# Kernel tuning notes

Measured on AMD Instinct MI355X. Metric: run time of the kernel, lower is better.

Reference implementation:

```python
import jax, jax.numpy as jnp
import numpy as np

EPS = 1e-15

def gmm_conv(x, row, col, pseudo, g_w, mu, sigma, root_w, bias):
    # x: [N,Fin], pseudo: [E,D], g_w: [Fin,K*Fout], mu/sigma: [K,D], root_w: [Fin,Fout]
    N = x.shape[0]
    K, D = mu.shape
    Fout = g_w.shape[1] // K
    gx = (x @ g_w).reshape(N, K, Fout)                       # per-node kernel transforms
    diff = pseudo[:, None, :] - mu[None, :, :]               # [E,K,D]
    gauss = jnp.exp(-0.5 * jnp.sum(diff * diff / (EPS + sigma[None] ** 2), axis=-1))  # [E,K]
    msg = jnp.einsum('ek,eko->eo', gauss, gx[row])           # [E,Fout]
    agg = jax.ops.segment_sum(msg, col, num_segments=N)      # scatter-add to targets
    cnt = jax.ops.segment_sum(jnp.ones((msg.shape[0],), x.dtype), col, num_segments=N)
    agg = agg / jnp.maximum(cnt, 1.0)[:, None]               # mean aggregation (GMMConv default)
    return agg + x @ root_w + bias

def setup_inputs() -> dict:
    key = jax.random.key(0)
    ks = jax.random.split(key, 12)
    N, E, F, H, C, K, D = 50000, 800000, 128, 64, 16, 8, 2
    return {
        'x': jax.random.normal(ks[0], (N, F), jnp.float32),
        'edge_index': jax.random.randint(ks[1], (2, E), 0, N, jnp.int64),
        'edge_attr': jax.random.uniform(ks[2], (E, D), jnp.float32),
        'g1_w': jax.random.normal(ks[3], (F, K * H), jnp.float32) * 0.1,
        'mu1': jax.random.normal(ks[4], (K, D), jnp.float32),
        'sigma1': jax.random.uniform(ks[5], (K, D), jnp.float32) + 0.5,
        'root1_w': jax.random.normal(ks[6], (F, H), jnp.float32) * 0.1,
        'bias1': jnp.zeros((H,), jnp.float32),
        'g2_w': jax.random.normal(ks[7], (H, K * C), jnp.float32) * 0.1,
        'mu2': jax.random.normal(ks[8], (K, D), jnp.float32),
        'sigma2': jax.random.uniform(ks[9], (K, D), jnp.float32) + 0.5,
        'root2_w': jax.random.normal(ks[10], (H, C), jnp.float32) * 0.1,
        'bias2': jnp.zeros((C,), jnp.float32),
    }

def reference(x, edge_index, edge_attr, g1_w, mu1, sigma1, root1_w, bias1,
              g2_w, mu2, sigma2, root2_w, bias2):
    row, col = edge_index[0], edge_index[1]
    # dropout p applied in eval mode -> identity
    h = jax.nn.elu(gmm_conv(x, row, col, edge_attr, g1_w, mu1, sigma1, root1_w, bias1))
    out = gmm_conv(h, row, col, edge_attr, g2_w, mu2, sigma2, root2_w, bias2)
    return jax.nn.log_softmax(out, axis=1)
```

## Files before the change

### kernel.cpp

```cpp
#include <hip/hip_runtime.h>
#include <hip/hip_bf16.h>
#include <hip/hip_fp16.h>
#include <math.h>


#define NF 128
#define NH 64
#define NC 16
#define Z1NODES 16
#define Z1CAP 448
#define E2NODES 16
#define E2CAP 448
#define GXST 160

typedef __bf16 v8bf __attribute__((ext_vector_type(8)));
typedef float v4f __attribute__((ext_vector_type(4)));
typedef float v2f __attribute__((ext_vector_type(2)));

__device__ inline ushort f2bu(float x) {
  __hip_bfloat16 h = __float2bfloat16(x);
  return *(ushort*)&h;
}
__device__ inline v8bf ld_frag(const ushort* p) {
  uint4 u = *(const uint4*)p;
  return __builtin_bit_cast(v8bf, u);
}
__device__ inline v2f fma2(float w, v2f f, v2f a) {
  return __builtin_elementwise_fma((v2f){w, w}, f, a);
}

__global__ __launch_bounds__(256) void setup_kernel(
    const int* __restrict__ col, const float* __restrict__ x,
    const float* __restrict__ g1w, const float* __restrict__ r1w,
    const float* __restrict__ g2w, const float* __restrict__ r2w,
    int* __restrict__ counts, int* __restrict__ rank,
    ushort* __restrict__ A1, ushort* __restrict__ W1t,
    ushort* __restrict__ G2pT, int* __restrict__ bagg,
    int E, int N, int bh, int bc, int bp) {
  const int b = blockIdx.x, t = threadIdx.x;
  if (b < bh) {
    int e = b * 256 + t;
    if (e < E) rank[e] = atomicAdd(&counts[col[e]], 1);
  } else if (b < bh + bc) {
    int idx = (b - bh) * 256 + t;
    if (idx < N * 32) {
      int n = idx >> 5, c4 = idx & 31;
      float4 v = ((const float4*)x)[idx];
      ushort4 o;
      o.x = f2bu(v.x); o.y = f2bu(v.y); o.z = f2bu(v.z); o.w = f2bu(v.w);
      *(ushort4*)(A1 + (size_t)n * 1152 + 1024 + c4 * 4) = o;
    }
  } else if (b < bh + bc + bp) {
    int i = (b - bh - bc) * 256 + t;
    if (i < 64 * 1152) {
      int h = i / 1152, j = i % 1152;
      float v = (j < 1024) ? g1w[(size_t)(j & 127) * 512 + (j >> 7) * 64 + h]
                           : r1w[(size_t)(j - 1024) * 64 + h];
      W1t[i] = f2bu(v);
    } else {
      int i2 = i - 64 * 1152;
      if (i2 < 144 * 64) {
        int cp = i2 / 64, f = i2 % 64;
        float v;
        if (cp < 128) {
          int kq = cp >> 5, rem = cp & 31;
          int o = rem >> 1, k = kq * 2 + (rem & 1);
          v = g2w[(size_t)f * 128 + k * 16 + o];
        } else {
          v = r2w[(size_t)f * 16 + (cp - 128)];
        }
        G2pT[i2] = f2bu(v);
      }
    }
  } else {
    if (t < 64) bagg[t] = 0;
  }
}

__global__ __launch_bounds__(256) void scan_kernel(
    const int* __restrict__ counts, int* __restrict__ starts,
    int* __restrict__ bagg, int NB) {
  __shared__ int wsum[4];
  __shared__ int s_pre;
  const int t = threadIdx.x, lane = t & 63, wv = t >> 6;
  const int b = blockIdx.x;
  int4 v = ((const int4*)counts)[b * 256 + t];
  int tsum = v.x + v.y + v.z + v.w;
  int inc = tsum;
  #pragma unroll
  for (int off = 1; off < 64; off <<= 1) {
    int u = __shfl_up(inc, off, 64);
    if (lane >= off) inc += u;
  }
  if (lane == 63) wsum[wv] = inc;
  __syncthreads();
  int agg = wsum[0] + wsum[1] + wsum[2] + wsum[3];
  if (t == 0) atomicExch(&bagg[b], agg + 1);
  __threadfence();
  int pre = 0;
  if (wv == 0) {
    if (t < b) {
      int val;
      do { val = atomicAdd(&bagg[t], 0); } while (val == 0);
      pre = val - 1;
    }
    #pragma unroll
    for (int off = 32; off >= 1; off >>= 1) pre += __shfl_xor(pre, off, 64);
    if (lane == 0) s_pre = pre;
  }
  __syncthreads();
  int wpre = 0;
  for (int j = 0; j < wv; ++j) wpre += wsum[j];
  int excl = s_pre + wpre + inc - tsum;
  int4 o;
  o.x = excl; o.y = o.x + v.x; o.z = o.y + v.y; o.w = o.z + v.z;
  ((int4*)starts)[b * 256 + t] = o;
}

__global__ __launch_bounds__(256) void fillrec_kernel(
    const int* __restrict__ row, const int* __restrict__ col,
    const int* __restrict__ rank, const int* __restrict__ starts,
    const float* __restrict__ eattr, uint4* __restrict__ rec, int E) {
  int e = blockIdx.x * 256 + threadIdx.x;
  if (e >= E) return;
  int pos = starts[col[e]] + rank[e];
  int r = row[e];
  float2 p = *(const float2*)(eattr + 2 * e);
  rec[pos] = make_uint4((uint)(r * 2304), __float_as_uint(p.x),
                        __float_as_uint(p.y), (uint)(r * 320));
}

__global__ __launch_bounds__(256) void z1_kernel(
    ushort* __restrict__ A1, const uint4* __restrict__ rec,
    const float* __restrict__ mu1, const float* __restrict__ sg1,
    const int* __restrict__ starts, int N) {
  __shared__ __align__(16) float lw[Z1CAP + 8][8];
  __shared__ int loff[Z1CAP + 8];
  __shared__ float prm[32];
  const int t = threadIdx.x, lane = t & 63, wv = t >> 6;
  const int base = (int)blockIdx.x * Z1NODES;
  const int S = starts[base];
  const int cl = min(starts[base + Z1NODES] - S, Z1CAP);
  if (t < 8) {
    float s0 = sg1[2 * t], s1 = sg1[2 * t + 1];
    prm[t] = -0.5f / (1e-15f + s0 * s0);
    prm[8 + t] = -0.5f / (1e-15f + s1 * s1);
    prm[16 + t] = mu1[2 * t];
    prm[24 + t] = mu1[2 * t + 1];
  }
  __syncthreads();
  for (int i = t; i < cl; i += 256) {
    uint4 rr = rec[S + i];
    loff[i] = (int)rr.x;
    float p0 = __uint_as_float(rr.y), p1 = __uint_as_float(rr.z);
    float w[8];
    #pragma unroll
    for (int k = 0; k < 8; ++k) {
      float d0 = p0 - prm[16 + k], d1 = p1 - prm[24 + k];
      w[k] = __expf(fmaf(d0 * d0, prm[k], d1 * d1 * prm[8 + k]));
    }
    *(float4*)&lw[i][0] = make_float4(w[0], w[1], w[2], w[3]);
    *(float4*)&lw[i][4] = make_float4(w[4], w[5], w[6], w[7]);
  }
  if (t < 8) {
    loff[cl + t] = 0;
    *(float4*)&lw[cl + t][0] = make_float4(0.f, 0.f, 0.f, 0.f);
    *(float4*)&lw[cl + t][4] = make_float4(0.f, 0.f, 0.f, 0.f);
  }
  __syncthreads();

  const char* xb = (const char*)(A1 + 1024) + (lane << 2);

  for (int i = 0; i < Z1NODES / 4; ++i) {
    const int n = base + wv * 4 + i;
    const int be = starts[n], ee = starts[n + 1];
    v2f A[8];
    #pragma unroll
    for (int k = 0; k < 8; ++k) A[k] = (v2f){0.f, 0.f};

    const int reRel = min(ee - S, cl);
    for (int q = min(be - S, cl); q < reRel; q += 8) {
      int off[8];
      #pragma unroll
      for (int u = 0; u < 8; ++u) off[u] = loff[q + u];
      uint g[8];
      #pragma unroll
      for (int u = 0; u < 8; ++u) g[u] = *(const uint*)(xb + off[u]);
      #pragma unroll
      for (int u = 0; u < 8; ++u) {
        const bool ok = (q + u) < reRel;
        float4 wl = *(float4*)&lw[q + u][0];
        float4 wh = *(float4*)&lw[q + u][4];
        v2f F;
        F.x = ok ? __uint_as_float(g[u] << 16) : 0.f;
        F.y = ok ? __uint_as_float(g[u] & 0xffff0000u) : 0.f;
        A[0] = fma2(wl.x, F, A[0]);
        A[1] = fma2(wl.y, F, A[1]);
        A[2] = fma2(wl.z, F, A[2]);
        A[3] = fma2(wl.w, F, A[3]);
        A[4] = fma2(wh.x, F, A[4]);
        A[5] = fma2(wh.y, F, A[5]);
        A[6] = fma2(wh.z, F, A[6]);
        A[7] = fma2(wh.w, F, A[7]);
      }
    }
    const float inv = 1.f / fmaxf((float)(ee - be), 1.f);
    ushort* zr = A1 + (size_t)n * 1152;
    #pragma unroll
    for (int k = 0; k < 8; ++k) {
      uint pk = (uint)f2bu(A[k].x * inv) | ((uint)f2bu(A[k].y * inv) << 16);
      *(uint*)(zr + k * 128 + 2 * lane) = pk;
    }
  }
}

__global__ __launch_bounds__(256) void gemm12_kernel(
    const ushort* __restrict__ A1, const ushort* __restrict__ W1t,
    const float* __restrict__ b1, const ushort* __restrict__ G2pT,
    ushort* __restrict__ gx2e, int N) {
  __shared__ __align__(16) ushort As[2][64 * 32];
  __shared__ __align__(16) ushort Bs[2][64 * 32];
  __shared__ __align__(16) ushort Hs[64][72];
  const int t = threadIdx.x, lane = t & 63, wv = t >> 6;
  const int mfrag = lane & 15, quad = lane >> 4;
  const int m0 = (int)blockIdx.x * 64;
  const int st_r = t >> 2, st_c = (t & 3) * 8;
  const int st_o = st_r * 32 + st_c;
  const ushort* ag = A1 + (size_t)(m0 + st_r) * 1152 + st_c;
  const ushort* bg = W1t + (size_t)st_r * 1152 + st_c;

  {
    uint4 a0 = *(const uint4*)ag;
    uint4 b0 = *(const uint4*)bg;
    *(uint4*)(&As[0][st_o]) = a0;
    *(uint4*)(&Bs[0][st_o]) = b0;
  }
  __syncthreads();

  v4f acc[4];
  #pragma unroll
  for (int ct = 0; ct < 4; ++ct) acc[ct] = (v4f){0.f, 0.f, 0.f, 0.f};

  for (int kc = 0; kc < 36; ++kc) {
    const int cb = kc & 1, nb = cb ^ 1;
    uint4 an, bn;
    if (kc < 35) {
      an = *(const uint4*)(ag + (kc + 1) * 32);
      bn = *(const uint4*)(bg + (kc + 1) * 32);
    }
    v8bf a = ld_frag(&As[cb][(wv * 16 + mfrag) * 32 + quad * 8]);
    #pragma unroll
    for (int ct = 0; ct < 4; ++ct) {
      v8bf b = ld_frag(&Bs[cb][(ct * 16 + mfrag) * 32 + quad * 8]);
      acc[ct] = __builtin_amdgcn_mfma_f32_16x16x32_bf16(a, b, acc[ct], 0, 0, 0);
    }
    if (kc < 35) {
      *(uint4*)(&As[nb][st_o]) = an;
      *(uint4*)(&Bs[nb][st_o]) = bn;
      __syncthreads();
    }
  }
  #pragma unroll
  for (int ct = 0; ct < 4; ++ct) {
    const int colh = ct * 16 + mfrag;
    const float bc = b1[colh];
    #pragma unroll
    for (int r = 0; r < 4; ++r) {
      float v = acc[ct][r] + bc;
      v = v > 0.f ? v : expm1f(v);
      Hs[wv * 16 + quad * 4 + r][colh] = f2bu(v);
    }
  }
  __syncthreads();

  v4f acc2[9];
  #pragma unroll
  for (int t9 = 0; t9 < 9; ++t9) acc2[t9] = (v4f){0.f, 0.f, 0.f, 0.f};
  const ushort* brow = G2pT + (size_t)mfrag * 64 + quad * 8;
  #pragma unroll
  for (int kc = 0; kc < 2; ++kc) {
    v8bf a = ld_frag(&Hs[wv * 16 + mfrag][quad * 8 + kc * 32]);
    #pragma unroll
    for (int t9 = 0; t9 < 9; ++t9) {
      v8bf b = ld_frag(brow + (size_t)t9 * 16 * 64 + kc * 32);
      acc2[t9] = __builtin_amdgcn_mfma_f32_16x16x32_bf16(a, b, acc2[t9], 0, 0, 0);
    }
  }
  #pragma unroll
  for (int t9 = 0; t9 < 9; ++t9) {
    #pragma unroll
    for (int r = 0; r < 4; ++r) {
      int node = m0 + wv * 16 + quad * 4 + r;
      if (node < N)
        gx2e[(size_t)node * GXST + t9 * 16 + mfrag] = f2bu(acc2[t9][r]);
    }
  }
}

__global__ __launch_bounds__(256) void edge2_kernel(
    const ushort* __restrict__ gx2e, const uint4* __restrict__ rec,
    const float* __restrict__ mu2, const float* __restrict__ sg2,
    const int* __restrict__ starts, const float* __restrict__ b2,
    float* __restrict__ out, int N) {
  __shared__ __align__(16) float lw[E2CAP + 8][8];
  __shared__ int loff[E2CAP + 8];
  __shared__ float lb2[16];
  __shared__ float prm[32];
  const int t = threadIdx.x, lane = t & 63, wv = t >> 6;
  const int base = (int)blockIdx.x * E2NODES;
  const int S = starts[base];
  const int cl = min(starts[base + E2NODES] - S, E2CAP);
  if (t < 16) lb2[t] = b2[t];
  if (t < 8) {
    float s0 = sg2[2 * t], s1 = sg2[2 * t + 1];
    prm[t] = -0.5f / (1e-15f + s0 * s0);
    prm[8 + t] = -0.5f / (1e-15f + s1 * s1);
    prm[16 + t] = mu2[2 * t];
    prm[24 + t] = mu2[2 * t + 1];
  }
  __syncthreads();
  for (int i = t; i < cl; i += 256) {
    uint4 rr = rec[S + i];
    loff[i] = (int)rr.w;
    float p0 = __uint_as_float(rr.y), p1 = __uint_as_float(rr.z);
    float w[8];
    #pragma unroll
    for (int k = 0; k < 8; ++k) {
      float d0 = p0 - prm[16 + k], d1 = p1 - prm[24 + k];
      w[k] = __expf(fmaf(d0 * d0, prm[k], d1 * d1 * prm[8 + k]));
    }
    *(float4*)&lw[i][0] = make_float4(w[0], w[1], w[2], w[3]);
    *(float4*)&lw[i][4] = make_float4(w[4], w[5], w[6], w[7]);
  }
  if (t < 8) {
    loff[cl + t] = 0;
    *(float4*)&lw[cl + t][0] = make_float4(0.f, 0.f, 0.f, 0.f);
    *(float4*)&lw[cl + t][4] = make_float4(0.f, 0.f, 0.f, 0.f);
  }
  __syncthreads();

  const int o = lane & 15, kq = lane >> 4;
  const char* gb = (const char*)gx2e + kq * 64 + o * 4;

  for (int i = 0; i < E2NODES / 4; ++i) {
    const int n = base + wv * 4 + i;
    if (n >= N) continue;
    const int be = starts[n], ee = starts[n + 1];
    v2f ACC = (v2f){0.f, 0.f};
    const int reRel = min(ee - S, cl);
    for (int q = min(be - S, cl); q < reRel; q += 8) {
      int off[8];
      #pragma unroll
      for (int u = 0; u < 8; ++u) off[u] = loff[q + u];
      uint g[8];
      #pragma unroll
      for (int u = 0; u < 8; ++u) g[u] = *(const uint*)(gb + off[u]);
      #pragma unroll
      for (int u = 0; u < 8; ++u) {
        const bool ok = (q + u) < reRel;
        v2f W = *(v2f*)&lw[q + u][kq * 2];
        v2f F;
        F.x = ok ? __uint_as_float(g[u] << 16) : 0.f;
        F.y = ok ? __uint_as_float(g[u] & 0xffff0000u) : 0.f;
        ACC = __builtin_elementwise_fma(W, F, ACC);
      }
    }
    float s = ACC.x + ACC.y;
    s += __shfl_xor(s, 16, 64);
    s += __shfl_xor(s, 32, 64);
    const float inv = 1.f / fmaxf((float)(ee - be), 1.f);
    ushort ru = *((const ushort*)gx2e + (size_t)n * GXST + 128 + o);
    float root = __uint_as_float(((uint)ru) << 16);
    float v = s * inv + root + lb2[o];
    float mx = v;
    #pragma unroll
    for (int off = 8; off >= 1; off >>= 1) mx = fmaxf(mx, __shfl_xor(mx, off, 64));
    float sm = __expf(v - mx);
    #pragma unroll
    for (int off = 8; off >= 1; off >>= 1) sm += __shfl_xor(sm, off, 64);
    if (kq == 0) out[(size_t)n * NC + o] = v - mx - __logf(sm);
  }
}

extern "C" void kernel_launch(void* const* d_in, const int* in_sizes, int n_in,
                              void* d_out, int out_size, void* d_ws, size_t ws_size,
                              hipStream_t stream) {
  const float* x     = (const float*)d_in[0];
  const int*   eidx  = (const int*)d_in[1];
  const float* eattr = (const float*)d_in[2];
  const float* g1w   = (const float*)d_in[3];
  const float* mu1   = (const float*)d_in[4];
  const float* sg1   = (const float*)d_in[5];
  const float* r1w   = (const float*)d_in[6];
  const float* b1    = (const float*)d_in[7];
  const float* g2w   = (const float*)d_in[8];
  const float* mu2   = (const float*)d_in[9];
  const float* sg2   = (const float*)d_in[10];
  const float* r2w   = (const float*)d_in[11];
  const float* b2    = (const float*)d_in[12];

  const int N = in_sizes[0] / NF;
  const int E = in_sizes[1] / 2;
  const int* row = eidx;
  const int* col = eidx + E;
  const int N2 = (N + 63) & ~63;
  const int NP = (N + 1023) & ~1023;
  const int NB = NP / 1024;

  char* wsb = (char*)d_ws;
  uint4* rec   = (uint4*)wsb;
  ushort* gx2e = (ushort*)(wsb + (size_t)E * 16);
  ushort* A1   = gx2e + (size_t)N2 * GXST;
  ushort* W1t  = A1 + (size_t)N2 * 1152;
  ushort* G2pT = W1t + (size_t)64 * 1152;
  int* rank    = (int*)(G2pT + (size_t)144 * 64);
  int* counts  = rank + (size_t)E;
  int* starts  = counts + NP;
  int* bagg    = starts + NP;

  const int bh = (E + 255) / 256;
  const int bc = (N * 32 + 255) / 256;
  const int bp = (64 * 1152 + 144 * 64 + 255) / 256;

  hipMemsetAsync(counts, 0, (size_t)NP * sizeof(int), stream);
  setup_kernel<<<bh + bc + bp + 1, 256, 0, stream>>>(
      col, x, g1w, r1w, g2w, r2w, counts, rank, A1, W1t, G2pT, bagg,
      E, N, bh, bc, bp);
  scan_kernel<<<NB, 256, 0, stream>>>(counts, starts, bagg, NB);
  fillrec_kernel<<<bh, 256, 0, stream>>>(row, col, rank, starts, eattr, rec, E);
  z1_kernel<<<N / Z1NODES, 256, 0, stream>>>(A1, rec, mu1, sg1, starts, N);
  gemm12_kernel<<<N2 / 64, 256, 0, stream>>>(A1, W1t, b1, G2pT, gx2e, N);
  edge2_kernel<<<(N + E2NODES - 1) / E2NODES, 256, 0, stream>>>(
      gx2e, rec, mu2, sg2, starts, b2, (float*)d_out, N);
}
```

Before: 286.9 us.

## Fuse layer-1 aggregation with both GEMMs in shared memory

```diff
diff --git a/kernel.cpp b/kernel.cpp
--- a/kernel.cpp
+++ b/kernel.cpp
@@ -8,10 +8,11 @@
 #define NH 64
 #define NC 16
 #define Z1NODES 16
-#define Z1CAP 448
+#define Z1CAP 432
 #define E2NODES 16
 #define E2CAP 448
 #define GXST 160
+#define ZTST 1160
 
 typedef __bf16 v8bf __attribute__((ext_vector_type(8)));
 typedef float v4f __attribute__((ext_vector_type(4)));
@@ -34,7 +35,7 @@
     const float* __restrict__ g1w, const float* __restrict__ r1w,
     const float* __restrict__ g2w, const float* __restrict__ r2w,
     int* __restrict__ counts, int* __restrict__ rank,
-    ushort* __restrict__ A1, ushort* __restrict__ W1t,
+    ushort* __restrict__ x_bf, ushort* __restrict__ W1t,
     ushort* __restrict__ G2pT, int* __restrict__ bagg,
     int E, int N, int bh, int bc, int bp) {
   const int b = blockIdx.x, t = threadIdx.x;
@@ -48,7 +49,7 @@
       float4 v = ((const float4*)x)[idx];
       ushort4 o;
       o.x = f2bu(v.x); o.y = f2bu(v.y); o.z = f2bu(v.z); o.w = f2bu(v.w);
-      *(ushort4*)(A1 + (size_t)n * 1152 + 1024 + c4 * 4) = o;
+      *(ushort4*)(x_bf + (size_t)n * 128 + c4 * 4) = o;
     }
   } else if (b < bh + bc + bp) {
     int i = (b - bh - bc) * 256 + t;
@@ -126,21 +127,29 @@
   int pos = starts[col[e]] + rank[e];
   int r = row[e];
   float2 p = *(const float2*)(eattr + 2 * e);
-  rec[pos] = make_uint4((uint)(r * 2304), __float_as_uint(p.x),
+  rec[pos] = make_uint4((uint)(r * 256), __float_as_uint(p.x),
                         __float_as_uint(p.y), (uint)(r * 320));
 }
 
-__global__ __launch_bounds__(256) void z1_kernel(
-    ushort* __restrict__ A1, const uint4* __restrict__ rec,
+__global__ __launch_bounds__(256) void z1g_kernel(
+    const ushort* __restrict__ x_bf, const uint4* __restrict__ rec,
     const float* __restrict__ mu1, const float* __restrict__ sg1,
-    const int* __restrict__ starts, int N) {
-  __shared__ __align__(16) float lw[Z1CAP + 8][8];
-  __shared__ int loff[Z1CAP + 8];
-  __shared__ float prm[32];
+    const int* __restrict__ starts, const ushort* __restrict__ W1t,
+    const float* __restrict__ b1, const ushort* __restrict__ G2pT,
+    ushort* __restrict__ gx2e, int N) {
+  __shared__ __align__(16) char smA[15968];
+  __shared__ __align__(16) ushort Zt[16][ZTST];
+  float (*lw)[8] = reinterpret_cast<float(*)[8]>(smA);
+  int* loff      = reinterpret_cast<int*>(smA + 14080);
+  float* prm     = reinterpret_cast<float*>(smA + 14080 + 1760);
+  ushort (*Hs)[72] = reinterpret_cast<ushort(*)[72]>(smA);
+
   const int t = threadIdx.x, lane = t & 63, wv = t >> 6;
+  const int mfrag = lane & 15, quad = lane >> 4;
   const int base = (int)blockIdx.x * Z1NODES;
   const int S = starts[base];
   const int cl = min(starts[base + Z1NODES] - S, Z1CAP);
+
   if (t < 8) {
     float s0 = sg1[2 * t], s1 = sg1[2 * t + 1];
     prm[t] = -0.5f / (1e-15f + s0 * s0);
@@ -167,12 +176,18 @@
     *(float4*)&lw[cl + t][0] = make_float4(0.f, 0.f, 0.f, 0.f);
     *(float4*)&lw[cl + t][4] = make_float4(0.f, 0.f, 0.f, 0.f);
   }
-  __syncthreads();
-
-  const char* xb = (const char*)(A1 + 1024) + (lane << 2);
+  {
+    int rr = t >> 4, cc = t & 15;
+    uint4 v = *(const uint4*)(x_bf + (size_t)(base + rr) * 128 + cc * 8);
+    *(uint4*)(&Zt[rr][1024 + cc * 8]) = v;
+  }
+  __syncthreads();
+
+  const char* xb = (const char*)x_bf + (lane << 2);
 
   for (int i = 0; i < Z1NODES / 4; ++i) {
     const int n = base + wv * 4 + i;
+    const int nl = wv * 4 + i;
     const int be = starts[n], ee = starts[n + 1];
     v2f A[8];
     #pragma unroll
@@ -205,94 +220,48 @@
       }
     }
     const float inv = 1.f / fmaxf((float)(ee - be), 1.f);
-    ushort* zr = A1 + (size_t)n * 1152;
+    ushort* zr = &Zt[nl][0];
     #pragma unroll
     for (int k = 0; k < 8; ++k) {
       uint pk = (uint)f2bu(A[k].x * inv) | ((uint)f2bu(A[k].y * inv) << 16);
       *(uint*)(zr + k * 128 + 2 * lane) = pk;
     }
   }
-}
-
-__global__ __launch_bounds__(256) void gemm12_kernel(
-    const ushort* __restrict__ A1, const ushort* __restrict__ W1t,
-    const float* __restrict__ b1, const ushort* __restrict__ G2pT,
-    ushort* __restrict__ gx2e, int N) {
-  __shared__ __align__(16) ushort As[2][64 * 32];
-  __shared__ __align__(16) ushort Bs[2][64 * 32];
-  __shared__ __align__(16) ushort Hs[64][72];
-  const int t = threadIdx.x, lane = t & 63, wv = t >> 6;
-  const int mfrag = lane & 15, quad = lane >> 4;
-  const int m0 = (int)blockIdx.x * 64;
-  const int st_r = t >> 2, st_c = (t & 3) * 8;
-  const int st_o = st_r * 32 + st_c;
-  const ushort* ag = A1 + (size_t)(m0 + st_r) * 1152 + st_c;
-  const ushort* bg = W1t + (size_t)st_r * 1152 + st_c;
-
+  __syncthreads();
+
+  v4f hacc = (v4f){0.f, 0.f, 0.f, 0.f};
+  const ushort* wrow = W1t + (size_t)(wv * 16 + mfrag) * 1152 + quad * 8;
+  #pragma unroll 4
+  for (int kc = 0; kc < 36; ++kc) {
+    v8bf a = ld_frag(&Zt[mfrag][quad * 8 + kc * 32]);
+    v8bf b = ld_frag(wrow + kc * 32);
+    hacc = __builtin_amdgcn_mfma_f32_16x16x32_bf16(a, b, hacc, 0, 0, 0);
+  }
   {
-    uint4 a0 = *(const uint4*)ag;
-    uint4 b0 = *(const uint4*)bg;
-    *(uint4*)(&As[0][st_o]) = a0;
-    *(uint4*)(&Bs[0][st_o]) = b0;
-  }
-  __syncthreads();
-
-  v4f acc[4];
-  #pragma unroll
-  for (int ct = 0; ct < 4; ++ct) acc[ct] = (v4f){0.f, 0.f, 0.f, 0.f};
-
-  for (int kc = 0; kc < 36; ++kc) {
-    const int cb = kc & 1, nb = cb ^ 1;
-    uint4 an, bn;
-    if (kc < 35) {
-      an = *(const uint4*)(ag + (kc + 1) * 32);
-      bn = *(const uint4*)(bg + (kc + 1) * 32);
-    }
-    v8bf a = ld_frag(&As[cb][(wv * 16 + mfrag) * 32 + quad * 8]);
-    #pragma unroll
-    for (int ct = 0; ct < 4; ++ct) {
-      v8bf b = ld_frag(&Bs[cb][(ct * 16 + mfrag) * 32 + quad * 8]);
-      acc[ct] = __builtin_amdgcn_mfma_f32_16x16x32_bf16(a, b, acc[ct], 0, 0, 0);
-    }
-    if (kc < 35) {
-      *(uint4*)(&As[nb][st_o]) = an;
-      *(uint4*)(&Bs[nb][st_o]) = bn;
-      __syncthreads();
-    }
-  }
-  #pragma unroll
-  for (int ct = 0; ct < 4; ++ct) {
-    const int colh = ct * 16 + mfrag;
+    const int colh = wv * 16 + mfrag;
     const float bc = b1[colh];
     #pragma unroll
     for (int r = 0; r < 4; ++r) {
-      float v = acc[ct][r] + bc;
+      float v = hacc[r] + bc;
       v = v > 0.f ? v : expm1f(v);
-      Hs[wv * 16 + quad * 4 + r][colh] = f2bu(v);
-    }
-  }
-  __syncthreads();
-
-  v4f acc2[9];
-  #pragma unroll
-  for (int t9 = 0; t9 < 9; ++t9) acc2[t9] = (v4f){0.f, 0.f, 0.f, 0.f};
-  const ushort* brow = G2pT + (size_t)mfrag * 64 + quad * 8;
-  #pragma unroll
-  for (int kc = 0; kc < 2; ++kc) {
-    v8bf a = ld_frag(&Hs[wv * 16 + mfrag][quad * 8 + kc * 32]);
-    #pragma unroll
-    for (int t9 = 0; t9 < 9; ++t9) {
-      v8bf b = ld_frag(brow + (size_t)t9 * 16 * 64 + kc * 32);
-      acc2[t9] = __builtin_amdgcn_mfma_f32_16x16x32_bf16(a, b, acc2[t9], 0, 0, 0);
-    }
-  }
-  #pragma unroll
-  for (int t9 = 0; t9 < 9; ++t9) {
+      Hs[quad * 4 + r][colh] = f2bu(v);
+    }
+  }
+  __syncthreads();
+
+  for (int t9 = wv; t9 < 9; t9 += 4) {
+    v4f acc2 = (v4f){0.f, 0.f, 0.f, 0.f};
+    const ushort* brow = G2pT + (size_t)(t9 * 16 + mfrag) * 64 + quad * 8;
+    #pragma unroll
+    for (int kc = 0; kc < 2; ++kc) {
+      v8bf a = ld_frag(&Hs[mfrag][quad * 8 + kc * 32]);
+      v8bf b = ld_frag(brow + kc * 32);
+      acc2 = __builtin_amdgcn_mfma_f32_16x16x32_bf16(a, b, acc2, 0, 0, 0);
+    }
     #pragma unroll
     for (int r = 0; r < 4; ++r) {
-      int node = m0 + wv * 16 + quad * 4 + r;
-      if (node < N)
-        gx2e[(size_t)node * GXST + t9 * 16 + mfrag] = f2bu(acc2[t9][r]);
+      int node = base + quad * 4 + r;
+      gx2e[(size_t)node * GXST + t9 * 16 + mfrag] = f2bu(acc2[r]);
     }
   }
 }
@@ -410,8 +379,8 @@
   char* wsb = (char*)d_ws;
   uint4* rec   = (uint4*)wsb;
   ushort* gx2e = (ushort*)(wsb + (size_t)E * 16);
-  ushort* A1   = gx2e + (size_t)N2 * GXST;
-  ushort* W1t  = A1 + (size_t)N2 * 1152;
+  ushort* x_bf = gx2e + (size_t)N2 * GXST;
+  ushort* W1t  = x_bf + (size_t)N2 * 128;
   ushort* G2pT = W1t + (size_t)64 * 1152;
   int* rank    = (int*)(G2pT + (size_t)144 * 64);
   int* counts  = rank + (size_t)E;
@@ -424,12 +393,12 @@
 
   hipMemsetAsync(counts, 0, (size_t)NP * sizeof(int), stream);
   setup_kernel<<<bh + bc + bp + 1, 256, 0, stream>>>(
-      col, x, g1w, r1w, g2w, r2w, counts, rank, A1, W1t, G2pT, bagg,
+      col, x, g1w, r1w, g2w, r2w, counts, rank, x_bf, W1t, G2pT, bagg,
       E, N, bh, bc, bp);
   scan_kernel<<<NB, 256, 0, stream>>>(counts, starts, bagg, NB);
   fillrec_kernel<<<bh, 256, 0, stream>>>(row, col, rank, starts, eattr, rec, E);
-  z1_kernel<<<N / Z1NODES, 256, 0, stream>>>(A1, rec, mu1, sg1, starts, N);
-  gemm12_kernel<<<N2 / 64, 256, 0, stream>>>(A1, W1t, b1, G2pT, gx2e, N);
+  z1g_kernel<<<N / Z1NODES, 256, 0, stream>>>(x_bf, rec, mu1, sg1, starts,
+                                              W1t, b1, G2pT, gx2e, N);
   edge2_kernel<<<(N + E2NODES - 1) / E2NODES, 256, 0, stream>>>(
       gx2e, rec, mu2, sg2, starts, b2, (float*)d_out, N);
 }
```

New measurement: 294.4 us. 2.6% more time.
